# Kernel tuning notes

Hardware: AMD Instinct MI355X
Metric: run time of the kernel (lower is better)

## Reference

```python
import jax, jax.numpy as jnp
import numpy as np

QN, QP = -8.0, 7.0  # int4: Qn=-2**3, Qp=2**3-1
LOG2E = 1.4426950408889634  # 1/ln(2)

def round_ste(x):
    return x + jax.lax.stop_gradient(jnp.round(x) - x)

def sg(x):
    return jax.lax.stop_gradient(x)

def mean_var_int(x_int, scale=1024):
    """Serial integer running-mean/var recurrence over the last dim.
    x_int: (B,H,N,D) int32. Returns mu (int values, float32) and varn float32, shape (B,H,N,1).
    Matches the torch loop: m_i = m_{i-1} + (x_i-m_{i-1})*int(1024/(i+1))//1024,
    v_i = v_{i-1} + (x_i-m_{i-1})*(x_i-m_i), with m_0=x_0, v_0=0 (same as the general
    recurrence with m_{-1}=v_{-1}=0 since int(1024/1)=1024)."""
    D = x_int.shape[3]
    coef = jnp.array([scale // (i + 1) for i in range(D)], dtype=jnp.int32)
    xt = jnp.moveaxis(x_int, 3, 0)  # (D,B,H,N)
    z = jnp.zeros(x_int.shape[:3], jnp.int32)
    def step(carry, inp):
        m, v = carry
        xi, c = inp
        d = xi - m
        new_m = m + (d * c) // scale  # floor division, matches torch //
        new_v = v + d * (xi - new_m)
        return (new_m, new_v), None
    (m, v), _ = jax.lax.scan(step, (z, z), (xt, coef))
    mu = m[..., None].astype(jnp.float32)
    varn = v[..., None].astype(jnp.float32) / D
    return mu, varn

def q_attention_forward(x0, qkv_w, qkv_b, qkv_alpha, qkv_act_alpha,
                        proj_w, proj_b, proj_alpha, proj_act_alpha,
                        norm_q_w, norm_q_b, norm_k_w, norm_k_b,
                        q_alpha, k_alpha, v_alpha, attn_alpha,
                        num_heads=12):
    B, N, C = x0.shape
    H = num_heads
    hd = C // H
    head_scale = hd ** -0.5

    # input activation quantization (ActQ_v2 then .int())
    a_in = qkv_act_alpha.mean()
    x0_2b = sg(jnp.round(jnp.clip(x0 / a_in, QN, QP)))  # int-valued (B,N,C)

    # int4 qkv weight quantization (per-output-channel alpha), integer GEMM
    w_qkv = sg(jnp.round(jnp.clip(qkv_w / qkv_alpha[:, None], QN, QP)))  # (3C,C)
    qkv = jnp.einsum('bnc,oc->bno', x0_2b, w_qkv)
    bias_i = sg(jnp.trunc(qkv_b / a_in / qkv_alpha))  # bias.int()
    qkv = qkv + bias_i

    qkv = jnp.transpose(qkv.reshape(B, N, 3, H, hd), (2, 0, 3, 1, 4))
    q0, k0, v0 = qkv[0], qkv[1], qkv[2]  # (B,H,N,hd)
    alpha_r = qkv_alpha.reshape(3, H, 1, hd)

    # q branch: scaled integer mean/var norm + scaled quantization
    xq = q0 * alpha_r[0]
    mu_q, var_q = mean_var_int(xq.astype(jnp.int32))
    q1 = (xq - mu_q) / (jnp.sqrt(var_q) + 1e-5)
    aq = q_alpha.mean()
    q2 = sg(jnp.round(jnp.clip((q1 + norm_q_b / norm_q_w) * norm_q_w / aq, QN, QP)))

    # k branch
    xk = k0 * alpha_r[1]
    mu_k, var_k = mean_var_int(xk.astype(jnp.int32))
    k1 = (xk - mu_k) / (jnp.sqrt(var_k) + 1e-5)
    ak = k_alpha.mean()
    k2 = sg(jnp.round(jnp.clip((k1 + norm_k_b / norm_k_w) * norm_k_w / ak, QN, QP)))

    # v branch
    av = v_alpha.mean()
    v2 = sg(jnp.round(jnp.clip(v0 * (a_in * alpha_r[2]) / av, QN, QP)))

    # integer q @ k^T
    qk = jnp.einsum('bhqd,bhkd->bhqk', q2, k2)  # (B,H,N,N)

    # power-of-two softmax approximation: 2^floor(e) * (1 + frac(e))
    s = head_scale * aq * ak
    e = LOG2E * s * qk
    f = jnp.floor(e)
    attn_exp = jnp.exp2(f) * (1.0 + (e - f))
    am = attn_alpha.mean()
    attn_norm = attn_exp / attn_exp.sum(-1, keepdims=True)
    attn2 = sg(jnp.round(jnp.clip(attn_norm / am, QN, QP)))

    x1p = jnp.einsum('bhqk,bhkd->bhqd', attn2, v2)
    x1p = jnp.transpose(x1p, (0, 2, 1, 3)).reshape(B, N, C)

    # proj-act quantization (round_pass STE, no .int() here in torch)
    ap = proj_act_alpha.mean()
    x1_2b = round_ste(jnp.clip(x1p * (am * av) / ap, QN, QP))

    w_p = sg(jnp.round(jnp.clip(proj_w / proj_alpha[:, None], QN, QP)))  # w_q.int()
    x2 = jnp.einsum('bnc,oc->bno', x1_2b, w_p) * proj_alpha * ap + proj_b
    return x2

def setup_inputs() -> dict:
    key = jax.random.key(0)
    ks = jax.random.split(key, 17)
    B, N, C, H = 4, 1024, 768, 12
    u = lambda k, shape, lo, hi: jax.random.uniform(k, shape, jnp.float32, lo, hi)
    return {
        "x0": jax.random.normal(ks[0], (B, N, C), jnp.float32),
        "qkv_w": jax.random.normal(ks[1], (3 * C, C), jnp.float32) * 0.02,
        "qkv_b": jax.random.normal(ks[2], (3 * C,), jnp.float32),
        "qkv_alpha": u(ks[3], (3 * C,), 0.008, 0.012),
        "qkv_act_alpha": u(ks[4], (C,), 0.25, 0.35),
        "proj_w": jax.random.normal(ks[5], (C, C), jnp.float32) * 0.02,
        "proj_b": jax.random.normal(ks[6], (C,), jnp.float32) * 0.02,
        "proj_alpha": u(ks[7], (C,), 0.008, 0.012),
        "proj_act_alpha": u(ks[8], (C,), 0.008, 0.012),
        "norm_q_w": u(ks[9], (C // H,), 0.8, 1.2),
        "norm_q_b": jax.random.normal(ks[10], (C // H,), jnp.float32) * 0.1,
        "norm_k_w": u(ks[11], (C // H,), 0.8, 1.2),
        "norm_k_b": jax.random.normal(ks[12], (C // H,), jnp.float32) * 0.1,
        "q_alpha": u(ks[13], (H,), 0.25, 0.35),
        "k_alpha": u(ks[14], (H,), 0.25, 0.35),
        "v_alpha": u(ks[15], (H,), 0.15, 0.25),
        "attn_alpha": u(ks[16], (H,), 0.0008, 0.0015),
    }

def reference(x0, qkv_w, qkv_b, qkv_alpha, qkv_act_alpha,
              proj_w, proj_b, proj_alpha, proj_act_alpha,
              norm_q_w, norm_q_b, norm_k_w, norm_k_b,
              q_alpha, k_alpha, v_alpha, attn_alpha):
    return q_attention_forward(x0, qkv_w, qkv_b, qkv_alpha, qkv_act_alpha,
                               proj_w, proj_b, proj_alpha, proj_act_alpha,
                               norm_q_w, norm_q_b, norm_k_w, norm_k_b,
                               q_alpha, k_alpha, v_alpha, attn_alpha)
```

## Files before the change

### kernel.cpp

```cpp
#include <hip/hip_runtime.h>

typedef unsigned short u16;
typedef unsigned int u32;
typedef __attribute__((ext_vector_type(8))) u16 u16x8;
typedef __attribute__((ext_vector_type(8))) __bf16 bf16x8;
typedef __attribute__((ext_vector_type(4))) float f32x4;

#define LOG2E_F 1.4426950408889634f

__device__ __forceinline__ u16 f2bf(float f) {
  return (u16)(__float_as_uint(f) >> 16);
}
__device__ __forceinline__ float clip87(float x) {
  return fminf(fmaxf(x, -8.0f), 7.0f);
}

typedef const __attribute__((address_space(1))) u32* gp32;
typedef __attribute__((address_space(3))) u32* lp32;
__device__ __forceinline__ void gl16(const void* g, void* l) {
  __builtin_amdgcn_global_load_lds((gp32)g, (lp32)l, 16, 0, 0);
}

__global__ void k_scalars(const float* __restrict__ qkv_act_alpha,
                          const float* __restrict__ proj_act_alpha,
                          const float* __restrict__ q_alpha,
                          const float* __restrict__ k_alpha,
                          const float* __restrict__ v_alpha,
                          const float* __restrict__ attn_alpha,
                          float* __restrict__ scal) {
  int tid = threadIdx.x;
  int wave = tid >> 6, lane = tid & 63;
  if (wave < 6) {
    const float* src = nullptr; int n = 0;
    switch (wave) {
      case 0: src = qkv_act_alpha;  n = 768; break;
      case 1: src = q_alpha;        n = 12;  break;
      case 2: src = k_alpha;        n = 12;  break;
      case 3: src = v_alpha;        n = 12;  break;
      case 4: src = attn_alpha;     n = 12;  break;
      case 5: src = proj_act_alpha; n = 768; break;
    }
    double s = 0.0;
    for (int i = lane; i < n; i += 64) s += (double)src[i];
    s += __shfl_xor(s, 1);
    s += __shfl_xor(s, 2);
    s += __shfl_xor(s, 4);
    s += __shfl_xor(s, 8);
    s += __shfl_xor(s, 16);
    s += __shfl_xor(s, 32);
    if (lane == 0) scal[wave] = (float)(s / (double)n);
  }
  __syncthreads();
  if (tid == 0) {
    float aq = scal[1], ak = scal[2];
    float s_ = (0.125f * aq) * ak;
    scal[6] = LOG2E_F * s_;
    scal[7] = scal[4] * scal[3];
  }
}

__global__ __launch_bounds__(256) void k_quant_weights(
    const float* __restrict__ qkv_w, const float* __restrict__ qkv_alpha,
    const float* __restrict__ qkv_b, const float* __restrict__ proj_w,
    const float* __restrict__ proj_alpha, const float* __restrict__ scal,
    u16* __restrict__ wq, u16* __restrict__ wp, float* __restrict__ biasi) {
  int idx = blockIdx.x * 256 + threadIdx.x;
  const int T1 = 2304 * 768, T2 = 768 * 768;
  if (idx < T1) {
    int o = idx / 768;
    wq[idx] = f2bf(rintf(clip87(qkv_w[idx] / qkv_alpha[o])));
  } else if (idx < T1 + T2) {
    int j = idx - T1;
    int o = j / 768;
    wp[j] = f2bf(rintf(clip87(proj_w[j] / proj_alpha[o])));
  } else if (idx < T1 + T2 + 2304) {
    int o = idx - T1 - T2;
    biasi[o] = truncf((qkv_b[o] / scal[0]) / qkv_alpha[o]);
  }
}

__global__ __launch_bounds__(256) void k_quant_x0(const float* __restrict__ x0,
                                                  const float* __restrict__ scal,
                                                  u16* __restrict__ x0q) {
  int base = (blockIdx.x * 256 + threadIdx.x) * 8;
  float a = scal[0];
  f32x4 v0 = *(const f32x4*)&x0[base];
  f32x4 v1 = *(const f32x4*)&x0[base + 4];
  u16x8 o;
  #pragma unroll
  for (int j = 0; j < 4; j++) o[j] = f2bf(rintf(clip87(v0[j] / a)));
  #pragma unroll
  for (int j = 0; j < 4; j++) o[4 + j] = f2bf(rintf(clip87(v1[j] / a)));
  *(u16x8*)&x0q[base] = o;
}

#define BUF_A(c) (smem_u16 + (c) * 8192)
#define BUF_B(c) (smem_u16 + 16384 + (c) * 8192)

__device__ __forceinline__ void stage_tile(const u16* gAl, const u16* gBl, int K,
                                           u16* bufA, u16* bufB, int w) {
  #pragma unroll
  for (int i = 0; i < 4; i++)
    gl16(gAl + (size_t)(i * 8) * K, bufA + (w * 32 + i * 8) * 64);
  #pragma unroll
  for (int i = 0; i < 4; i++)
    gl16(gBl + (size_t)(i * 8) * K, bufB + (w * 32 + i * 8) * 64);
}

__device__ __forceinline__ void gemm_steps(const u16* __restrict__ A,
                                           const u16* __restrict__ Bt, int K,
                                           int m0, int n0, u16* smem_u16,
                                           int lane, int wave, f32x4 acc[4][4]) {
  int rsub = lane >> 3;
  int jsrc = (lane & 7) ^ rsub;
  const u16* gAl = A + (size_t)(m0 + wave * 32 + rsub) * K + jsrc * 8;
  const u16* gBl = Bt + (size_t)(n0 + wave * 32 + rsub) * K + jsrc * 8;

  int arow = (wave >> 1) * 64 + (lane & 15);
  int brow = (wave & 1) * 64 + (lane & 15);
  int nsteps = K / 64;

  stage_tile(gAl, gBl, K, BUF_A(0), BUF_B(0), wave);
  __syncthreads();
  for (int t = 0; t < nsteps; t++) {
    int cur = t & 1;
    if (t + 1 < nsteps)
      stage_tile(gAl + (t + 1) * 64, gBl + (t + 1) * 64, K,
                 BUF_A(cur ^ 1), BUF_B(cur ^ 1), wave);
    const u16* bA = BUF_A(cur);
    const u16* bB = BUF_B(cur);
    #pragma unroll
    for (int kk = 0; kk < 2; kk++) {
      int jj = ((kk * 4 + (lane >> 4)) ^ (lane & 7)) * 8;
      bf16x8 af[4], bf[4];
      #pragma unroll
      for (int mi = 0; mi < 4; mi++) af[mi] = *(const bf16x8*)&bA[(arow + mi * 16) * 64 + jj];
      #pragma unroll
      for (int ni = 0; ni < 4; ni++) bf[ni] = *(const bf16x8*)&bB[(brow + ni * 16) * 64 + jj];
      #pragma unroll
      for (int mi = 0; mi < 4; mi++)
        #pragma unroll
        for (int ni = 0; ni < 4; ni++)
          acc[mi][ni] = __builtin_amdgcn_mfma_f32_16x16x32_bf16(af[mi], bf[ni], acc[mi][ni], 0, 0, 0);
    }
    __syncthreads();
  }
}

__global__ __launch_bounds__(256) void k_gemm_qkv(
    const u16* __restrict__ A, const u16* __restrict__ Bt,
    const float* __restrict__ biasi, const float* __restrict__ qkv_alpha,
    const float* __restrict__ nqw, const float* __restrict__ nqb,
    const float* __restrict__ nkw, const float* __restrict__ nkb,
    const float* __restrict__ scal,
    u16* __restrict__ q2, u16* __restrict__ k2, u16* __restrict__ v2t) {
  const int K = 768;
  __shared__ __align__(16) char smem[128 * 129 * 4];
  u16* smem_u16 = (u16*)smem;
  float* xt = (float*)smem;
  int tid = threadIdx.x;
  int lane = tid & 63, wave = tid >> 6;
  int wr = wave >> 1, wc = wave & 1;
  int m0 = blockIdx.y * 128, n0 = blockIdx.x * 128;

  f32x4 acc[4][4];
  #pragma unroll
  for (int mi = 0; mi < 4; mi++)
    #pragma unroll
    for (int ni = 0; ni < 4; ni++) acc[mi][ni] = (f32x4){0.f, 0.f, 0.f, 0.f};

  gemm_steps(A, Bt, K, m0, n0, smem_u16, lane, wave, acc);

  int lrow = (lane >> 4) * 4, lcol = lane & 15;
  #pragma unroll
  for (int mi = 0; mi < 4; mi++)
    #pragma unroll
    for (int ni = 0; ni < 4; ni++) {
      int c = wc * 64 + ni * 16 + lcol;
      float bs = biasi[n0 + c];
      #pragma unroll
      for (int rr = 0; rr < 4; rr++) {
        int r = wr * 64 + mi * 16 + lrow + rr;
        xt[r * 129 + c] = acc[mi][ni][rr] + bs;
      }
    }
  __syncthreads();

  int branch = blockIdx.x / 6, hp = blockIdx.x % 6;
  int b = m0 >> 10, nb = m0 & 1023;
  if (branch == 2) {
    int c = tid & 127, hf = tid >> 7;
    int h = hp * 2 + (c >> 6), d = c & 63;
    float av = scal[3];
    float coefv = scal[0] * qkv_alpha[1536 + h * 64 + d];
    u16* dst = v2t + ((size_t)(b * 12 + h) * 64 + d) * 1024 + nb + hf * 64;
    #pragma unroll
    for (int g = 0; g < 8; g++) {
      u16x8 t8;
      #pragma unroll
      for (int j = 0; j < 8; j++) {
        float val = xt[(hf * 64 + g * 8 + j) * 129 + c];
        t8[j] = f2bf(rintf(clip87((val * coefv) / av)));
      }
      *(u16x8*)(dst + g * 8) = t8;
    }
  } else {
    int r = tid & 127, hs = tid >> 7;
    int h = hp * 2 + hs;
    const float* alph = qkv_alpha + branch * 768 + h * 64;
    const float* wv = branch == 0 ? nqw : nkw;
    const float* bv = branch == 0 ? nqb : nkb;
    float as = branch == 0 ? scal[1] : scal[2];
    float xq[64];
    #pragma unroll
    for (int d = 0; d < 64; d++) xq[d] = xt[r * 129 + hs * 64 + d] * alph[d];
    int m = 0, v = 0;
    #pragma unroll
    for (int i = 0; i < 64; i++) {
      int xi = (int)xq[i];
      int dd = xi - m;
      m += (dd * (1024 / (i + 1))) >> 10;
      v += dd * (xi - m);
    }
    float muf = (float)m;
    float den = sqrtf((float)v * 0.015625f) + 1e-5f;
    u16* outp = (branch == 0 ? q2 : k2) + ((size_t)(b * 12 + h) * 1024 + nb + r) * 64;
    #pragma unroll
    for (int g = 0; g < 8; g++) {
      u16x8 t8;
      #pragma unroll
      for (int j = 0; j < 8; j++) {
        int d = g * 8 + j;
        float q1 = (xq[d] - muf) / den;
        float bw = bv[d] / wv[d];
        float t = (q1 + bw) * wv[d] / as;
        t8[j] = f2bf(rintf(clip87(t)));
      }
      *(u16x8*)(outp + g * 8) = t8;
    }
  }
}

__global__ __launch_bounds__(256) void k_gemm_proj(
    const u16* __restrict__ A, const u16* __restrict__ Bt,
    float* __restrict__ Cout, const float* __restrict__ palpha,
    const float* __restrict__ pbias, const float* __restrict__ scal) {
  const int K = 768, N = 768;
  __shared__ __align__(16) char smem[65536];
  u16* smem_u16 = (u16*)smem;
  int tid = threadIdx.x;
  int lane = tid & 63, wave = tid >> 6;
  int wr = wave >> 1, wc = wave & 1;
  int m0 = blockIdx.y * 128, n0 = blockIdx.x * 128;

  f32x4 acc[4][4];
  #pragma unroll
  for (int mi = 0; mi < 4; mi++)
    #pragma unroll
    for (int ni = 0; ni < 4; ni++) acc[mi][ni] = (f32x4){0.f, 0.f, 0.f, 0.f};

  gemm_steps(A, Bt, K, m0, n0, smem_u16, lane, wave, acc);

  int lrow = (lane >> 4) * 4, lcol = lane & 15;
  float ap = scal[5];
  #pragma unroll
  for (int mi = 0; mi < 4; mi++)
    #pragma unroll
    for (int ni = 0; ni < 4; ni++) {
      int col = n0 + wc * 64 + ni * 16 + lcol;
      float pa = palpha[col], pb = pbias[col];
      #pragma unroll
      for (int rr = 0; rr < 4; rr++) {
        int row = m0 + wr * 64 + mi * 16 + lrow + rr;
        Cout[(size_t)row * N + col] = (acc[mi][ni][rr] * pa) * ap + pb;
      }
    }
}

__global__ __launch_bounds__(256) void k_attn(
    const u16* __restrict__ q2, const u16* __restrict__ k2,
    const u16* __restrict__ v2t, const float* __restrict__ scal,
    u16* __restrict__ x1q) {
  __shared__ __align__(16) u16 lK[64 * 72];
  __shared__ __align__(16) u16 lV[64 * 72];
  __shared__ __align__(16) u16 lP[64 * 72];
  __shared__ float rs_lds[64];
  int tid = threadIdx.x, lane = tid & 63, wave = tid >> 6;
  int qt = blockIdx.x, bh = blockIdx.y;
  const float escale = scal[6], am = scal[4], am_av = scal[7], apc = scal[5];

  size_t qrow = (size_t)bh * 1024 + qt * 64 + wave * 16 + (lane & 15);
  bf16x8 qf0 = *(const bf16x8*)(q2 + qrow * 64 + (lane >> 4) * 8);
  bf16x8 qf1 = *(const bf16x8*)(q2 + qrow * 64 + 32 + (lane >> 4) * 8);

  const u16* k2b = k2 + (size_t)bh * 1024 * 64;
  const u16* v2b = v2t + (size_t)bh * 64 * 1024;
  int sr = tid >> 2, sc = (tid & 3) * 16;

  double rsum[4] = {0.0, 0.0, 0.0, 0.0};
  for (int kt = 0; kt < 16; kt++) {
    const u16* src = k2b + (size_t)(kt * 64 + sr) * 64 + sc;
    *(u16x8*)&lK[sr * 72 + sc]     = *(const u16x8*)src;
    *(u16x8*)&lK[sr * 72 + sc + 8] = *(const u16x8*)(src + 8);
    __syncthreads();
    float part[4] = {0.f, 0.f, 0.f, 0.f};
    #pragma unroll
    for (int ct = 0; ct < 4; ct++) {
      bf16x8 kf0 = *(const bf16x8*)&lK[(ct * 16 + (lane & 15)) * 72 + (lane >> 4) * 8];
      bf16x8 kf1 = *(const bf16x8*)&lK[(ct * 16 + (lane & 15)) * 72 + 32 + (lane >> 4) * 8];
      f32x4 s = {0.f, 0.f, 0.f, 0.f};
      s = __builtin_amdgcn_mfma_f32_16x16x32_bf16(qf0, kf0, s, 0, 0, 0);
      s = __builtin_amdgcn_mfma_f32_16x16x32_bf16(qf1, kf1, s, 0, 0, 0);
      #pragma unroll
      for (int rr = 0; rr < 4; rr++) {
        float e = escale * s[rr];
        float f = floorf(e);
        float pe = ldexpf(1.0f + (e - f), (int)f);
        part[rr] += pe;
      }
    }
    #pragma unroll
    for (int rr = 0; rr < 4; rr++) rsum[rr] += (double)part[rr];
    __syncthreads();
  }
  #pragma unroll
  for (int rr = 0; rr < 4; rr++) {
    double s = rsum[rr];
    s += __shfl_xor(s, 1);
    s += __shfl_xor(s, 2);
    s += __shfl_xor(s, 4);
    s += __shfl_xor(s, 8);
    if ((lane & 15) == 0) rs_lds[wave * 16 + (lane >> 4) * 4 + rr] = (float)s;
  }
  __syncthreads();
  float fac[4];
  #pragma unroll
  for (int rr = 0; rr < 4; rr++)
    fac[rr] = 1.0f / (rs_lds[wave * 16 + (lane >> 4) * 4 + rr] * am);

  f32x4 accv[4];
  #pragma unroll
  for (int ct = 0; ct < 4; ct++) accv[ct] = (f32x4){0.f, 0.f, 0.f, 0.f};

  for (int kt = 0; kt < 16; kt++) {
    const u16* srcK = k2b + (size_t)(kt * 64 + sr) * 64 + sc;
    *(u16x8*)&lK[sr * 72 + sc]     = *(const u16x8*)srcK;
    *(u16x8*)&lK[sr * 72 + sc + 8] = *(const u16x8*)(srcK + 8);
    const u16* srcV = v2b + (size_t)sr * 1024 + kt * 64 + sc;
    *(u16x8*)&lV[sr * 72 + sc]     = *(const u16x8*)srcV;
    *(u16x8*)&lV[sr * 72 + sc + 8] = *(const u16x8*)(srcV + 8);
    __syncthreads();
    #pragma unroll
    for (int ct = 0; ct < 4; ct++) {
      bf16x8 kf0 = *(const bf16x8*)&lK[(ct * 16 + (lane & 15)) * 72 + (lane >> 4) * 8];
      bf16x8 kf1 = *(const bf16x8*)&lK[(ct * 16 + (lane & 15)) * 72 + 32 + (lane >> 4) * 8];
      f32x4 s = {0.f, 0.f, 0.f, 0.f};
      s = __builtin_amdgcn_mfma_f32_16x16x32_bf16(qf0, kf0, s, 0, 0, 0);
      s = __builtin_amdgcn_mfma_f32_16x16x32_bf16(qf1, kf1, s, 0, 0, 0);
      #pragma unroll
      for (int rr = 0; rr < 4; rr++) {
        float e = escale * s[rr];
        float f = floorf(e);
        float pe = ldexpf(1.0f + (e - f), (int)f);
        float a2 = rintf(fminf(pe * fac[rr], 7.0f));
        lP[(wave * 16 + (lane >> 4) * 4 + rr) * 72 + ct * 16 + (lane & 15)] = f2bf(a2);
      }
    }
    __syncthreads();
    bf16x8 pf0 = *(const bf16x8*)&lP[(wave * 16 + (lane & 15)) * 72 + (lane >> 4) * 8];
    bf16x8 pf1 = *(const bf16x8*)&lP[(wave * 16 + (lane & 15)) * 72 + 32 + (lane >> 4) * 8];
    #pragma unroll
    for (int ct = 0; ct < 4; ct++) {
      bf16x8 vf0 = *(const bf16x8*)&lV[(ct * 16 + (lane & 15)) * 72 + (lane >> 4) * 8];
      bf16x8 vf1 = *(const bf16x8*)&lV[(ct * 16 + (lane & 15)) * 72 + 32 + (lane >> 4) * 8];
      accv[ct] = __builtin_amdgcn_mfma_f32_16x16x32_bf16(pf0, vf0, accv[ct], 0, 0, 0);
      accv[ct] = __builtin_amdgcn_mfma_f32_16x16x32_bf16(pf1, vf1, accv[ct], 0, 0, 0);
    }
    __syncthreads();
  }

  int b = bh / 12, h = bh % 12;
  #pragma unroll
  for (int ct = 0; ct < 4; ct++)
    #pragma unroll
    for (int rr = 0; rr < 4; rr++) {
      int qr = qt * 64 + wave * 16 + (lane >> 4) * 4 + rr;
      int col = h * 64 + ct * 16 + (lane & 15);
      float t = (accv[ct][rr] * am_av) / apc;
      x1q[((size_t)b * 1024 + qr) * 768 + col] = f2bf(rintf(clip87(t)));
    }
}

extern "C" void kernel_launch(void* const* d_in, const int* in_sizes, int n_in,
                              void* d_out, int out_size, void* d_ws, size_t ws_size,
                              hipStream_t stream) {
  const float* x0             = (const float*)d_in[0];
  const float* qkv_w          = (const float*)d_in[1];
  const float* qkv_b          = (const float*)d_in[2];
  const float* qkv_alpha      = (const float*)d_in[3];
  const float* qkv_act_alpha  = (const float*)d_in[4];
  const float* proj_w         = (const float*)d_in[5];
  const float* proj_b         = (const float*)d_in[6];
  const float* proj_alpha     = (const float*)d_in[7];
  const float* proj_act_alpha = (const float*)d_in[8];
  const float* nqw            = (const float*)d_in[9];
  const float* nqb            = (const float*)d_in[10];
  const float* nkw            = (const float*)d_in[11];
  const float* nkb            = (const float*)d_in[12];
  const float* q_alpha        = (const float*)d_in[13];
  const float* k_alpha        = (const float*)d_in[14];
  const float* v_alpha        = (const float*)d_in[15];
  const float* attn_alpha     = (const float*)d_in[16];
  float* out = (float*)d_out;

  char* ws = (char*)d_ws;
  size_t off = 0;
  auto alloc = [&](size_t bytes) -> void* {
    off = (off + 255) & ~(size_t)255;
    void* p = ws + off;
    off += bytes;
    return p;
  };
  float* scal = (float*)alloc(64);
  u16* wq     = (u16*)alloc((size_t)2304 * 768 * 2);
  u16* wp     = (u16*)alloc((size_t)768 * 768 * 2);
  float* biasi= (float*)alloc((size_t)2304 * 4);
  u16* x0q    = (u16*)alloc((size_t)4096 * 768 * 2);
  u16* q2     = (u16*)alloc((size_t)48 * 1024 * 64 * 2);
  u16* k2     = (u16*)alloc((size_t)48 * 1024 * 64 * 2);
  u16* v2t    = (u16*)alloc((size_t)48 * 1024 * 64 * 2);
  u16* x1q    = (u16*)alloc((size_t)4096 * 768 * 2);

  k_scalars<<<1, 384, 0, stream>>>(qkv_act_alpha, proj_act_alpha, q_alpha, k_alpha,
                                   v_alpha, attn_alpha, scal);

  int totW = 2304 * 768 + 768 * 768 + 2304;
  k_quant_weights<<<(totW + 255) / 256, 256, 0, stream>>>(qkv_w, qkv_alpha, qkv_b,
                                                          proj_w, proj_alpha, scal,
                                                          wq, wp, biasi);

  k_quant_x0<<<(4096 * 768) / (256 * 8), 256, 0, stream>>>(x0, scal, x0q);

  k_gemm_qkv<<<dim3(18, 32), 256, 0, stream>>>(x0q, wq, biasi, qkv_alpha,
                                               nqw, nqb, nkw, nkb, scal,
                                               q2, k2, v2t);

  k_attn<<<dim3(16, 48), 256, 0, stream>>>(q2, k2, v2t, scal, x1q);

  k_gemm_proj<<<dim3(6, 32), 256, 0, stream>>>(x1q, wp, out, proj_alpha, proj_b, scal);
}
```

Before: 212.7 us.

## Shrink QKV and projection GEMM tiles to 64x64 for more blocks

Both GEMM kernels move from 128x128 block tiles to 64x64 tiles, so the grids grow to 36x64 and 12x64 blocks. The aim is to fill more of the GPU's CUs and raise occupancy by cutting LDS use per block. The QKV epilogue now maps one head per block, and the serial mean/var recurrence runs on only 64 of the 256 threads. The cost is more global and LDS traffic per FLOP, since each tile is reused less, and three waves sit idle during the norm epilogue.

```diff
diff --git a/kernel.cpp b/kernel.cpp
--- a/kernel.cpp
+++ b/kernel.cpp
@@ -94,54 +94,50 @@
   *(u16x8*)&x0q[base] = o;
 }
 
-#define BUF_A(c) (smem_u16 + (c) * 8192)
-#define BUF_B(c) (smem_u16 + 16384 + (c) * 8192)
-
-__device__ __forceinline__ void stage_tile(const u16* gAl, const u16* gBl, int K,
-                                           u16* bufA, u16* bufB, int w) {
-  #pragma unroll
-  for (int i = 0; i < 4; i++)
-    gl16(gAl + (size_t)(i * 8) * K, bufA + (w * 32 + i * 8) * 64);
-  #pragma unroll
-  for (int i = 0; i < 4; i++)
-    gl16(gBl + (size_t)(i * 8) * K, bufB + (w * 32 + i * 8) * 64);
-}
-
-__device__ __forceinline__ void gemm_steps(const u16* __restrict__ A,
-                                           const u16* __restrict__ Bt, int K,
-                                           int m0, int n0, u16* smem_u16,
-                                           int lane, int wave, f32x4 acc[4][4]) {
+#define BUF_A64(c) (smem_u16 + (c) * 4096)
+#define BUF_B64(c) (smem_u16 + 8192 + (c) * 4096)
+
+__device__ __forceinline__ void stage64(const u16* gAl, const u16* gBl, int K,
+                                        u16* bufA, u16* bufB, int w) {
+  gl16(gAl, bufA + (w * 16) * 64);
+  gl16(gAl + (size_t)8 * K, bufA + (w * 16 + 8) * 64);
+  gl16(gBl, bufB + (w * 16) * 64);
+  gl16(gBl + (size_t)8 * K, bufB + (w * 16 + 8) * 64);
+}
+
+__device__ __forceinline__ void gemm64(const u16* __restrict__ A,
+                                       const u16* __restrict__ Bt, int K,
+                                       int m0, int n0, u16* smem_u16,
+                                       int lane, int wave, f32x4 acc[2][2]) {
   int rsub = lane >> 3;
   int jsrc = (lane & 7) ^ rsub;
-  const u16* gAl = A + (size_t)(m0 + wave * 32 + rsub) * K + jsrc * 8;
-  const u16* gBl = Bt + (size_t)(n0 + wave * 32 + rsub) * K + jsrc * 8;
-
-  int arow = (wave >> 1) * 64 + (lane & 15);
-  int brow = (wave & 1) * 64 + (lane & 15);
+  const u16* gAl = A + (size_t)(m0 + wave * 16 + rsub) * K + jsrc * 8;
+  const u16* gBl = Bt + (size_t)(n0 + wave * 16 + rsub) * K + jsrc * 8;
+
+  int arow = (wave >> 1) * 32 + (lane & 15);
+  int brow = (wave & 1) * 32 + (lane & 15);
   int nsteps = K / 64;
 
-  stage_tile(gAl, gBl, K, BUF_A(0), BUF_B(0), wave);
+  stage64(gAl, gBl, K, BUF_A64(0), BUF_B64(0), wave);
   __syncthreads();
   for (int t = 0; t < nsteps; t++) {
     int cur = t & 1;
     if (t + 1 < nsteps)
-      stage_tile(gAl + (t + 1) * 64, gBl + (t + 1) * 64, K,
-                 BUF_A(cur ^ 1), BUF_B(cur ^ 1), wave);
-    const u16* bA = BUF_A(cur);
-    const u16* bB = BUF_B(cur);
+      stage64(gAl + (t + 1) * 64, gBl + (t + 1) * 64, K,
+              BUF_A64(cur ^ 1), BUF_B64(cur ^ 1), wave);
+    const u16* bA = BUF_A64(cur);
+    const u16* bB = BUF_B64(cur);
     #pragma unroll
     for (int kk = 0; kk < 2; kk++) {
       int jj = ((kk * 4 + (lane >> 4)) ^ (lane & 7)) * 8;
-      bf16x8 af[4], bf[4];
-      #pragma unroll
-      for (int mi = 0; mi < 4; mi++) af[mi] = *(const bf16x8*)&bA[(arow + mi * 16) * 64 + jj];
-      #pragma unroll
-      for (int ni = 0; ni < 4; ni++) bf[ni] = *(const bf16x8*)&bB[(brow + ni * 16) * 64 + jj];
-      #pragma unroll
-      for (int mi = 0; mi < 4; mi++)
-        #pragma unroll
-        for (int ni = 0; ni < 4; ni++)
-          acc[mi][ni] = __builtin_amdgcn_mfma_f32_16x16x32_bf16(af[mi], bf[ni], acc[mi][ni], 0, 0, 0);
+      bf16x8 af0 = *(const bf16x8*)&bA[arow * 64 + jj];
+      bf16x8 af1 = *(const bf16x8*)&bA[(arow + 16) * 64 + jj];
+      bf16x8 bf0 = *(const bf16x8*)&bB[brow * 64 + jj];
+      bf16x8 bf1 = *(const bf16x8*)&bB[(brow + 16) * 64 + jj];
+      acc[0][0] = __builtin_amdgcn_mfma_f32_16x16x32_bf16(af0, bf0, acc[0][0], 0, 0, 0);
+      acc[0][1] = __builtin_amdgcn_mfma_f32_16x16x32_bf16(af0, bf1, acc[0][1], 0, 0, 0);
+      acc[1][0] = __builtin_amdgcn_mfma_f32_16x16x32_bf16(af1, bf0, acc[1][0], 0, 0, 0);
+      acc[1][1] = __builtin_amdgcn_mfma_f32_16x16x32_bf16(af1, bf1, acc[1][1], 0, 0, 0);
     }
     __syncthreads();
   }
@@ -155,65 +151,63 @@
     const float* __restrict__ scal,
     u16* __restrict__ q2, u16* __restrict__ k2, u16* __restrict__ v2t) {
   const int K = 768;
-  __shared__ __align__(16) char smem[128 * 129 * 4];
+  __shared__ __align__(16) char smem[32768];
   u16* smem_u16 = (u16*)smem;
   float* xt = (float*)smem;
   int tid = threadIdx.x;
   int lane = tid & 63, wave = tid >> 6;
   int wr = wave >> 1, wc = wave & 1;
-  int m0 = blockIdx.y * 128, n0 = blockIdx.x * 128;
-
-  f32x4 acc[4][4];
-  #pragma unroll
-  for (int mi = 0; mi < 4; mi++)
-    #pragma unroll
-    for (int ni = 0; ni < 4; ni++) acc[mi][ni] = (f32x4){0.f, 0.f, 0.f, 0.f};
-
-  gemm_steps(A, Bt, K, m0, n0, smem_u16, lane, wave, acc);
+  int m0 = blockIdx.y * 64, n0 = blockIdx.x * 64;
+
+  f32x4 acc[2][2];
+  #pragma unroll
+  for (int mi = 0; mi < 2; mi++)
+    #pragma unroll
+    for (int ni = 0; ni < 2; ni++) acc[mi][ni] = (f32x4){0.f, 0.f, 0.f, 0.f};
+
+  gemm64(A, Bt, K, m0, n0, smem_u16, lane, wave, acc);
 
   int lrow = (lane >> 4) * 4, lcol = lane & 15;
   #pragma unroll
-  for (int mi = 0; mi < 4; mi++)
-    #pragma unroll
-    for (int ni = 0; ni < 4; ni++) {
-      int c = wc * 64 + ni * 16 + lcol;
+  for (int mi = 0; mi < 2; mi++)
+    #pragma unroll
+    for (int ni = 0; ni < 2; ni++) {
+      int c = wc * 32 + ni * 16 + lcol;
       float bs = biasi[n0 + c];
       #pragma unroll
       for (int rr = 0; rr < 4; rr++) {
-        int r = wr * 64 + mi * 16 + lrow + rr;
-        xt[r * 129 + c] = acc[mi][ni][rr] + bs;
+        int r = wr * 32 + mi * 16 + lrow + rr;
+        xt[r * 65 + c] = acc[mi][ni][rr] + bs;
       }
     }
   __syncthreads();
 
-  int branch = blockIdx.x / 6, hp = blockIdx.x % 6;
+  int branch = blockIdx.x / 12, h = blockIdx.x % 12;
   int b = m0 >> 10, nb = m0 & 1023;
   if (branch == 2) {
-    int c = tid & 127, hf = tid >> 7;
-    int h = hp * 2 + (c >> 6), d = c & 63;
+    int d = tid & 63, qr = tid >> 6;
     float av = scal[3];
     float coefv = scal[0] * qkv_alpha[1536 + h * 64 + d];
-    u16* dst = v2t + ((size_t)(b * 12 + h) * 64 + d) * 1024 + nb + hf * 64;
-    #pragma unroll
-    for (int g = 0; g < 8; g++) {
+    u16* dst = v2t + ((size_t)(b * 12 + h) * 64 + d) * 1024 + nb + qr * 16;
+    #pragma unroll
+    for (int g = 0; g < 2; g++) {
       u16x8 t8;
       #pragma unroll
       for (int j = 0; j < 8; j++) {
-        float val = xt[(hf * 64 + g * 8 + j) * 129 + c];
+        float val = xt[(qr * 16 + g * 8 + j) * 65 + d];
         t8[j] = f2bf(rintf(clip87((val * coefv) / av)));
       }
       *(u16x8*)(dst + g * 8) = t8;
     }
-  } else {
-    int r = tid & 127, hs = tid >> 7;
-    int h = hp * 2 + hs;
+  } else if (tid < 64) {
+    int r = tid;
     const float* alph = qkv_alpha + branch * 768 + h * 64;
     const float* wv = branch == 0 ? nqw : nkw;
     const float* bv = branch == 0 ? nqb : nkb;
     float as = branch == 0 ? scal[1] : scal[2];
     float xq[64];
     #pragma unroll
-    for (int d = 0; d < 64; d++) xq[d] = xt[r * 129 + hs * 64 + d] * alph[d];
+    for (int d = 0; d < 64; d++) xq[d] = xt[r * 65 + d] * alph[d];
     int m = 0, v = 0;
     #pragma unroll
     for (int i = 0; i < 64; i++) {
@@ -246,32 +240,32 @@
     float* __restrict__ Cout, const float* __restrict__ palpha,
     const float* __restrict__ pbias, const float* __restrict__ scal) {
   const int K = 768, N = 768;
-  __shared__ __align__(16) char smem[65536];
+  __shared__ __align__(16) char smem[32768];
   u16* smem_u16 = (u16*)smem;
   int tid = threadIdx.x;
   int lane = tid & 63, wave = tid >> 6;
   int wr = wave >> 1, wc = wave & 1;
-  int m0 = blockIdx.y * 128, n0 = blockIdx.x * 128;
-
-  f32x4 acc[4][4];
-  #pragma unroll
-  for (int mi = 0; mi < 4; mi++)
-    #pragma unroll
-    for (int ni = 0; ni < 4; ni++) acc[mi][ni] = (f32x4){0.f, 0.f, 0.f, 0.f};
-
-  gemm_steps(A, Bt, K, m0, n0, smem_u16, lane, wave, acc);
+  int m0 = blockIdx.y * 64, n0 = blockIdx.x * 64;
+
+  f32x4 acc[2][2];
+  #pragma unroll
+  for (int mi = 0; mi < 2; mi++)
+    #pragma unroll
+    for (int ni = 0; ni < 2; ni++) acc[mi][ni] = (f32x4){0.f, 0.f, 0.f, 0.f};
+
+  gemm64(A, Bt, K, m0, n0, smem_u16, lane, wave, acc);
 
   int lrow = (lane >> 4) * 4, lcol = lane & 15;
   float ap = scal[5];
   #pragma unroll
-  for (int mi = 0; mi < 4; mi++)
-    #pragma unroll
-    for (int ni = 0; ni < 4; ni++) {
-      int col = n0 + wc * 64 + ni * 16 + lcol;
+  for (int mi = 0; mi < 2; mi++)
+    #pragma unroll
+    for (int ni = 0; ni < 2; ni++) {
+      int col = n0 + wc * 32 + ni * 16 + lcol;
       float pa = palpha[col], pb = pbias[col];
       #pragma unroll
       for (int rr = 0; rr < 4; rr++) {
-        int row = m0 + wr * 64 + mi * 16 + lrow + rr;
+        int row = m0 + wr * 32 + mi * 16 + lrow + rr;
         Cout[(size_t)row * N + col] = (acc[mi][ni][rr] * pa) * ap + pb;
       }
     }
@@ -441,11 +435,11 @@
 
   k_quant_x0<<<(4096 * 768) / (256 * 8), 256, 0, stream>>>(x0, scal, x0q);
 
-  k_gemm_qkv<<<dim3(18, 32), 256, 0, stream>>>(x0q, wq, biasi, qkv_alpha,
+  k_gemm_qkv<<<dim3(36, 64), 256, 0, stream>>>(x0q, wq, biasi, qkv_alpha,
                                                nqw, nqb, nkw, nkb, scal,
                                                q2, k2, v2t);
 
   k_attn<<<dim3(16, 48), 256, 0, stream>>>(q2, k2, v2t, scal, x1q);
 
-  k_gemm_proj<<<dim3(6, 32), 256, 0, stream>>>(x1q, wp, out, proj_alpha, proj_b, scal);
-}
+  k_gemm_proj<<<dim3(12, 64), 256, 0, stream>>>(x1q, wp, out, proj_alpha, proj_b, scal);
+}
```

Result: slower. 217.6 us (+2.3%).
